# Kernel tuning notes

Hardware: AMD Instinct MI355X
Metric: run time of the kernel (lower is better)

## Reference

```python
import jax, jax.numpy as jnp
import numpy as np

B, N, F, D, H = 4, 2048, 128, 128, 4

def setup_inputs() -> dict:
    key = jax.random.key(0)
    k1, k2, k3, k4 = jax.random.split(key, 4)
    X = jax.random.normal(k1, (B, N, F), dtype=jnp.float32)
    A = jax.random.uniform(k2, (B, N, N), dtype=jnp.float32)
    kernel = jax.random.normal(k3, (F, D), dtype=jnp.float32) * 0.05
    bias = jnp.ones((D,), dtype=jnp.float32)
    attn = jax.random.normal(k4, (H, D, D), dtype=jnp.float32) * 0.05
    return {"X": X, "A": A, "kernel": kernel, "bias": bias, "attn": attn}

def reference(X, A, kernel, bias, attn):
    # Linear projection: [B,N,F] @ [F,D] + bias -> [B,N,D]
    Xp = jnp.einsum('bnf,fd->bnd', X, kernel) + bias
    # Per-head bilinear scores Xp @ attn_h @ Xp^T, batched over heads: [B,H,N,N]
    scores = jnp.einsum('bnd,hde,bme->bhnm', Xp, attn, Xp)
    # Adjacency mask + tanh (fused elementwise)
    Am = jnp.tanh(A[:, None, :, :] * scores)
    # Weighted aggregate per head: [B,H,N,N] @ [B,N,D] -> [B,H,N,D]
    heads = jnp.einsum('bhnm,bmd->bhnd', Am, Xp)
    # Mean over heads, relu
    Xh = jax.nn.relu(jnp.mean(heads, axis=1))
    # Skip connection (shapes match since F == D): relu(Xh + X)
    out = jax.nn.relu(Xh + X)
    return out
```

## Files before the change

### kernel.cpp

```cpp
#include <hip/hip_runtime.h>

#define NB 4
#define NN 2048
#define ND 128
#define NH 4

typedef short short8 __attribute__((ext_vector_type(8)));
typedef short short4v __attribute__((ext_vector_type(4)));
typedef float floatx4 __attribute__((ext_vector_type(4)));

__device__ __forceinline__ short f2bf(float f){
  unsigned u = __float_as_uint(f);
  u += 0x7FFFu + ((u >> 16) & 1u);
  return (short)(u >> 16);
}
__device__ __forceinline__ float bf2f(short s){
  unsigned u = ((unsigned)(unsigned short)s) << 16;
  return __uint_as_float(u);
}

__global__ void k0_transpose(const float* __restrict__ W, const float* __restrict__ attn,
                             short* __restrict__ WT, short* __restrict__ attnT){
  int mat = blockIdx.x;
  const float* src = (mat == 0) ? W : (attn + (mat - 1) * 16384);
  short* dst = (mat == 0) ? WT : (attnT + (mat - 1) * 16384);
  __shared__ short tile[128 * 130];
  int t = threadIdx.x;
  for (int k = 0; k < 64; ++k){
    int idx = k * 256 + t;
    int r = idx >> 7, c = idx & 127;
    tile[c * 130 + r] = f2bf(src[idx]);
  }
  __syncthreads();
  for (int k = 0; k < 8; ++k){
    int g = k * 256 + t;
    int r = g >> 4, c8 = g & 15;
    short8 v;
    #pragma unroll
    for (int j = 0; j < 8; ++j) v[j] = tile[r * 130 + c8 * 8 + j];
    *(short8*)&dst[r * 128 + c8 * 8] = v;
  }
}

__global__ __launch_bounds__(256) void k1_xp(const float* __restrict__ X,
                                             const short* __restrict__ WT,
                                             const float* __restrict__ bias,
                                             short* __restrict__ Xp){
  int bid = blockIdx.x;
  int b = bid >> 5, i0 = (bid & 31) << 6;
  int t = threadIdx.x, w = t >> 6, lane = t & 63, lq = lane >> 4, lc = lane & 15;
  __shared__ __align__(16) short ldsB[16384];
  #pragma unroll
  for (int c = 0; c < 8; ++c){
    int q = c * 256 + t; int fblk = q >> 7; int d = q & 127;
    *(short8*)&ldsB[q * 8] = *(const short8*)&WT[d * 128 + fblk * 8];
  }
  short8 af[4][4];
  #pragma unroll
  for (int ib = 0; ib < 4; ++ib)
    #pragma unroll
    for (int k = 0; k < 4; ++k){
      const float* xp = &X[(b * NN + i0 + ib * 16 + lc) * ND + k * 32 + lq * 8];
      float4 x0 = *(const float4*)xp;
      float4 x1 = *(const float4*)(xp + 4);
      short8 s;
      s[0]=f2bf(x0.x); s[1]=f2bf(x0.y); s[2]=f2bf(x0.z); s[3]=f2bf(x0.w);
      s[4]=f2bf(x1.x); s[5]=f2bf(x1.y); s[6]=f2bf(x1.z); s[7]=f2bf(x1.w);
      af[ib][k] = s;
    }
  __syncthreads();
  floatx4 acc[4][2];
  #pragma unroll
  for (int ib = 0; ib < 4; ++ib)
    #pragma unroll
    for (int eb = 0; eb < 2; ++eb) acc[ib][eb] = (floatx4){0.f, 0.f, 0.f, 0.f};
  #pragma unroll
  for (int eb = 0; eb < 2; ++eb)
    #pragma unroll
    for (int k = 0; k < 4; ++k){
      short8 bf = *(short8*)&ldsB[(k * 4 + lq) * 1024 + (w * 32 + eb * 16 + lc) * 8];
      #pragma unroll
      for (int ib = 0; ib < 4; ++ib)
        acc[ib][eb] = __builtin_amdgcn_mfma_f32_16x16x32_bf16(af[ib][k], bf, acc[ib][eb], 0, 0, 0);
    }
  #pragma unroll
  for (int ib = 0; ib < 4; ++ib)
    #pragma unroll
    for (int eb = 0; eb < 2; ++eb){
      int d = w * 32 + eb * 16 + lc;
      float bv = bias[d];
      #pragma unroll
      for (int r = 0; r < 4; ++r){
        int n = i0 + ib * 16 + lq * 4 + r;
        Xp[(b * NN + n) * ND + d] = f2bf(acc[ib][eb][r] + bv);
      }
    }
}

__global__ void k1b_transpose(const short* __restrict__ Xp, short* __restrict__ XpT){
  int bid = blockIdx.x;
  int b = bid >> 6; int rem = bid & 63;
  int n0 = (rem >> 1) << 6, d0 = (rem & 1) << 6;
  __shared__ short tile[64 * 66];
  int t = threadIdx.x;
  #pragma unroll
  for (int c = 0; c < 2; ++c){
    int g = c * 256 + t; int r = g >> 3, c8 = g & 7;
    short8 v = *(const short8*)&Xp[(b * NN + n0 + r) * ND + d0 + c8 * 8];
    #pragma unroll
    for (int j = 0; j < 8; ++j) tile[(c8 * 8 + j) * 66 + r] = v[j];
  }
  __syncthreads();
  #pragma unroll
  for (int c = 0; c < 2; ++c){
    int g = c * 256 + t; int d = g >> 3, n8 = g & 7;
    short8 v;
    #pragma unroll
    for (int j = 0; j < 8; ++j) v[j] = tile[d * 66 + n8 * 8 + j];
    *(short8*)&XpT[(b * ND + d0 + d) * NN + n0 + n8 * 8] = v;
  }
}

__global__ __launch_bounds__(256) void k2_y(const short* __restrict__ Xp,
                                            const short* __restrict__ attnT,
                                            short* __restrict__ Y){
  int bid = blockIdx.x;
  int it = bid & 31, h = (bid >> 5) & 3, b = bid >> 7;
  int i0 = it << 6;
  int t = threadIdx.x, w = t >> 6, lane = t & 63, lq = lane >> 4, lc = lane & 15;
  __shared__ __align__(16) short ldsB[16384];
  const short* Bsrc = attnT + h * 16384;
  #pragma unroll
  for (int c = 0; c < 8; ++c){
    int q = c * 256 + t; int dblk = q >> 7; int e = q & 127;
    *(short8*)&ldsB[q * 8] = *(const short8*)&Bsrc[e * 128 + dblk * 8];
  }
  short8 af[4][4];
  #pragma unroll
  for (int ib = 0; ib < 4; ++ib)
    #pragma unroll
    for (int k = 0; k < 4; ++k)
      af[ib][k] = *(const short8*)&Xp[(b * NN + i0 + ib * 16 + lc) * ND + k * 32 + lq * 8];
  __syncthreads();
  floatx4 acc[4][2];
  #pragma unroll
  for (int ib = 0; ib < 4; ++ib)
    #pragma unroll
    for (int eb = 0; eb < 2; ++eb) acc[ib][eb] = (floatx4){0.f, 0.f, 0.f, 0.f};
  #pragma unroll
  for (int eb = 0; eb < 2; ++eb)
    #pragma unroll
    for (int k = 0; k < 4; ++k){
      short8 bf = *(short8*)&ldsB[(k * 4 + lq) * 1024 + (w * 32 + eb * 16 + lc) * 8];
      #pragma unroll
      for (int ib = 0; ib < 4; ++ib)
        acc[ib][eb] = __builtin_amdgcn_mfma_f32_16x16x32_bf16(af[ib][k], bf, acc[ib][eb], 0, 0, 0);
    }
  #pragma unroll
  for (int ib = 0; ib < 4; ++ib)
    #pragma unroll
    for (int eb = 0; eb < 2; ++eb){
      int e = w * 32 + eb * 16 + lc;
      #pragma unroll
      for (int r = 0; r < 4; ++r){
        int n = i0 + ib * 16 + lq * 4 + r;
        Y[((b * NH + h) * NN + n) * ND + e] = f2bf(acc[ib][eb][r]);
      }
    }
}

__global__ __launch_bounds__(256, 4) void k3_fused(const short* __restrict__ Xp,
                                                   const short* __restrict__ XpT,
                                                   const short* __restrict__ Y,
                                                   const float* __restrict__ A,
                                                   float* __restrict__ part){
  int bid = blockIdx.x;
  int it = bid & 127, b = (bid >> 7) & 3, ms = bid >> 9;
  int i0 = it << 4;
  int t = threadIdx.x, w = t >> 6, lane = t & 63, lq = lane >> 4, lc = lane & 15;

  __shared__ __align__(16) short ldsPh[2][1024];
  __shared__ __align__(16) short ldsPl[2][1024];

  short8 yf[4][4];
  #pragma unroll
  for (int h = 0; h < 4; ++h)
    #pragma unroll
    for (int k = 0; k < 4; ++k)
      yf[h][k] = *(const short8*)&Y[((b * NH + h) * NN + i0 + lc) * ND + k * 32 + lq * 8];

  floatx4 acc[2];
  acc[0] = (floatx4){0.f,0.f,0.f,0.f};
  acc[1] = (floatx4){0.f,0.f,0.f,0.f};

  const int mbase = ms << 9;
  const int poff = (w * 2 + (lq >> 1)) * 128 + lc * 8 + (lq & 1) * 4;
  const float* arow = &A[(size_t)(b * NN + i0 + lc) * NN];

  floatx4 av = *(const floatx4*)&arow[mbase + w * 16 + lq * 4];

  for (int itn = 0; itn < 8; ++itn){
    int p = itn & 1;
    int m0 = mbase + itn * 64;

    short8 xtf[2][2];
    #pragma unroll
    for (int kb = 0; kb < 2; ++kb)
      #pragma unroll
      for (int db = 0; db < 2; ++db)
        xtf[kb][db] = *(const short8*)&XpT[(b * ND + w * 32 + db * 16 + lc) * NN
                                           + m0 + (kb * 4 + lq) * 8];

    short8 xpf[4];
    const short* xr = Xp + (b * NN + m0 + w * 16 + lc) * ND;
    #pragma unroll
    for (int k = 0; k < 4; ++k) xpf[k] = *(const short8*)&xr[k * 32 + lq * 8];

    floatx4 avn = av;
    if (itn < 7) avn = *(const floatx4*)&arow[m0 + 64 + w * 16 + lq * 4];

    float psum[4] = {0.f, 0.f, 0.f, 0.f};
    #pragma unroll
    for (int h = 0; h < 4; ++h){
      floatx4 S = (floatx4){0.f,0.f,0.f,0.f};
      #pragma unroll
      for (int k = 0; k < 4; ++k)
        S = __builtin_amdgcn_mfma_f32_16x16x32_bf16(xpf[k], yf[h][k], S, 0, 0, 0);
      #pragma unroll
      for (int r = 0; r < 4; ++r){
        float x = av[r] * S[r];
        float e = __builtin_amdgcn_exp2f(x * 2.885390081777926f);
        psum[r] += 1.f - 2.f * __builtin_amdgcn_rcpf(e + 1.f);
      }
    }
    short4v hi4, lo4;
    #pragma unroll
    for (int r = 0; r < 4; ++r){
      float pb = 0.25f * psum[r];
      short h16 = f2bf(pb);
      hi4[r] = h16;
      lo4[r] = f2bf(pb - bf2f(h16));
    }
    *(short4v*)&ldsPh[p][poff] = hi4;
    *(short4v*)&ldsPl[p][poff] = lo4;
    __syncthreads();

    #pragma unroll
    for (int kb = 0; kb < 2; ++kb){
      short8 ph = *(short8*)&ldsPh[p][(kb * 4 + lq) * 128 + lc * 8];
      short8 pl = *(short8*)&ldsPl[p][(kb * 4 + lq) * 128 + lc * 8];
      #pragma unroll
      for (int db = 0; db < 2; ++db){
        acc[db] = __builtin_amdgcn_mfma_f32_16x16x32_bf16(ph, xtf[kb][db], acc[db], 0, 0, 0);
        acc[db] = __builtin_amdgcn_mfma_f32_16x16x32_bf16(pl, xtf[kb][db], acc[db], 0, 0, 0);
      }
    }
    av = avn;
  }
  float* dst = part + (size_t)ms * 1048576 + (b * NN + i0) * ND;
  #pragma unroll
  for (int db = 0; db < 2; ++db)
    #pragma unroll
    for (int r = 0; r < 4; ++r)
      dst[(lq * 4 + r) * ND + w * 32 + db * 16 + lc] = acc[db][r];
}

__global__ void k4_final(const float* __restrict__ part, const float* __restrict__ X,
                         float* __restrict__ out){
  int f = (blockIdx.x * 256 + threadIdx.x) * 4;
  float4 s0 = *(const float4*)(part + f);
  float4 s1 = *(const float4*)(part + 1048576 + f);
  float4 s2 = *(const float4*)(part + 2097152 + f);
  float4 s3 = *(const float4*)(part + 3145728 + f);
  float4 xv = *(const float4*)(X + f);
  float4 o;
  o.x = fmaxf(fmaxf(s0.x + s1.x + s2.x + s3.x, 0.f) + xv.x, 0.f);
  o.y = fmaxf(fmaxf(s0.y + s1.y + s2.y + s3.y, 0.f) + xv.y, 0.f);
  o.z = fmaxf(fmaxf(s0.z + s1.z + s2.z + s3.z, 0.f) + xv.z, 0.f);
  o.w = fmaxf(fmaxf(s0.w + s1.w + s2.w + s3.w, 0.f) + xv.w, 0.f);
  *(float4*)(out + f) = o;
}

extern "C" void kernel_launch(void* const* d_in, const int* in_sizes, int n_in,
                              void* d_out, int out_size, void* d_ws, size_t ws_size,
                              hipStream_t stream) {
  const float* X    = (const float*)d_in[0];
  const float* A    = (const float*)d_in[1];
  const float* W    = (const float*)d_in[2];
  const float* bias = (const float*)d_in[3];
  const float* attn = (const float*)d_in[4];
  float* out = (float*)d_out;

  const size_t OFF_XP    = 0;
  const size_t OFF_XPT   = (size_t)2 << 20;
  const size_t OFF_Y     = (size_t)4 << 20;
  const size_t OFF_PART  = (size_t)12 << 20;
  const size_t OFF_WT    = (size_t)28 << 20;
  const size_t OFF_ATTNT = OFF_WT + 32768;
  const size_t NEED = OFF_ATTNT + 131072;
  if (ws_size < NEED) return;

  char* ws = (char*)d_ws;
  short* Xp    = (short*)(ws + OFF_XP);
  short* XpT   = (short*)(ws + OFF_XPT);
  short* Y     = (short*)(ws + OFF_Y);
  float* part  = (float*)(ws + OFF_PART);
  short* WT    = (short*)(ws + OFF_WT);
  short* attnT = (short*)(ws + OFF_ATTNT);

  k0_transpose<<<5, 256, 0, stream>>>(W, attn, WT, attnT);
  k1_xp<<<128, 256, 0, stream>>>(X, WT, bias, Xp);
  k1b_transpose<<<256, 256, 0, stream>>>(Xp, XpT);
  k2_y<<<512, 256, 0, stream>>>(Xp, attnT, Y);
  k3_fused<<<2048, 256, 0, stream>>>(Xp, XpT, Y, A, part);
  k4_final<<<1024, 256, 0, stream>>>(part, X, out);
}
```

Measured before the change: 196.9 us.

## Remove per-iteration barrier by giving each wave all output columns

```diff
diff --git a/kernel.cpp b/kernel.cpp
--- a/kernel.cpp
+++ b/kernel.cpp
@@ -179,53 +179,51 @@
   int i0 = it << 4;
   int t = threadIdx.x, w = t >> 6, lane = t & 63, lq = lane >> 4, lc = lane & 15;
 
-  __shared__ __align__(16) short ldsPh[2][1024];
-  __shared__ __align__(16) short ldsPl[2][1024];
-
-  short8 yf[4][4];
-  #pragma unroll
-  for (int h = 0; h < 4; ++h)
-    #pragma unroll
-    for (int k = 0; k < 4; ++k)
-      yf[h][k] = *(const short8*)&Y[((b * NH + h) * NN + i0 + lc) * ND + k * 32 + lq * 8];
-
-  floatx4 acc[2];
-  acc[0] = (floatx4){0.f,0.f,0.f,0.f};
-  acc[1] = (floatx4){0.f,0.f,0.f,0.f};
+  __shared__ __align__(16) char smem[32768];
+
+  #pragma unroll
+  for (int c = 0; c < 4; ++c){
+    int slot = c * 256 + t;
+    int h = slot >> 8, i = (slot >> 4) & 15, d8 = slot & 15;
+    short8 v = *(const short8*)&Y[((b * NH + h) * NN + i0 + i) * ND + d8 * 8];
+    *(short8*)(smem + h * 4096 + i * 256 + ((d8 ^ (i & 7)) << 4)) = v;
+  }
+  __syncthreads();
+
+  floatx4 acc[8];
+  #pragma unroll
+  for (int dt = 0; dt < 8; ++dt) acc[dt] = (floatx4){0.f,0.f,0.f,0.f};
 
   const int mbase = ms << 9;
-  const int poff = (w * 2 + (lq >> 1)) * 128 + lc * 8 + (lq & 1) * 4;
   const float* arow = &A[(size_t)(b * NN + i0 + lc) * NN];
 
   floatx4 av = *(const floatx4*)&arow[mbase + w * 16 + lq * 4];
 
   for (int itn = 0; itn < 8; ++itn){
-    int p = itn & 1;
-    int m0 = mbase + itn * 64;
-
-    short8 xtf[2][2];
-    #pragma unroll
-    for (int kb = 0; kb < 2; ++kb)
-      #pragma unroll
-      for (int db = 0; db < 2; ++db)
-        xtf[kb][db] = *(const short8*)&XpT[(b * ND + w * 32 + db * 16 + lc) * NN
-                                           + m0 + (kb * 4 + lq) * 8];
+    int m0 = mbase + itn * 64 + w * 16;
 
     short8 xpf[4];
-    const short* xr = Xp + (b * NN + m0 + w * 16 + lc) * ND;
+    const short* xr = Xp + (b * NN + m0 + lc) * ND;
     #pragma unroll
     for (int k = 0; k < 4; ++k) xpf[k] = *(const short8*)&xr[k * 32 + lq * 8];
 
+    short4v xt[8];
+    #pragma unroll
+    for (int dt = 0; dt < 8; ++dt)
+      xt[dt] = *(const short4v*)&XpT[(size_t)(b * ND + dt * 16 + lc) * NN + m0 + lq * 4];
+
     floatx4 avn = av;
-    if (itn < 7) avn = *(const floatx4*)&arow[m0 + 64 + w * 16 + lq * 4];
+    if (itn < 7) avn = *(const floatx4*)&arow[m0 + 64 + lq * 4];
 
     float psum[4] = {0.f, 0.f, 0.f, 0.f};
     #pragma unroll
     for (int h = 0; h < 4; ++h){
       floatx4 S = (floatx4){0.f,0.f,0.f,0.f};
       #pragma unroll
-      for (int k = 0; k < 4; ++k)
-        S = __builtin_amdgcn_mfma_f32_16x16x32_bf16(xpf[k], yf[h][k], S, 0, 0, 0);
+      for (int k = 0; k < 4; ++k){
+        short8 yf = *(short8*)(smem + h * 4096 + lc * 256 + (((k * 4 + lq) ^ (lc & 7)) << 4));
+        S = __builtin_amdgcn_mfma_f32_16x16x32_bf16(xpf[k], yf, S, 0, 0, 0);
+      }
       #pragma unroll
       for (int r = 0; r < 4; ++r){
         float x = av[r] * S[r];
@@ -233,6 +231,7 @@
         psum[r] += 1.f - 2.f * __builtin_amdgcn_rcpf(e + 1.f);
       }
     }
+
     short4v hi4, lo4;
     #pragma unroll
     for (int r = 0; r < 4; ++r){
@@ -241,28 +240,29 @@
       hi4[r] = h16;
       lo4[r] = f2bf(pb - bf2f(h16));
     }
-    *(short4v*)&ldsPh[p][poff] = hi4;
-    *(short4v*)&ldsPl[p][poff] = lo4;
-    __syncthreads();
-
-    #pragma unroll
-    for (int kb = 0; kb < 2; ++kb){
-      short8 ph = *(short8*)&ldsPh[p][(kb * 4 + lq) * 128 + lc * 8];
-      short8 pl = *(short8*)&ldsPl[p][(kb * 4 + lq) * 128 + lc * 8];
-      #pragma unroll
-      for (int db = 0; db < 2; ++db){
-        acc[db] = __builtin_amdgcn_mfma_f32_16x16x32_bf16(ph, xtf[kb][db], acc[db], 0, 0, 0);
-        acc[db] = __builtin_amdgcn_mfma_f32_16x16x32_bf16(pl, xtf[kb][db], acc[db], 0, 0, 0);
-      }
+
+    #pragma unroll
+    for (int dt = 0; dt < 8; ++dt){
+      acc[dt] = __builtin_amdgcn_mfma_f32_16x16x16bf16_1k(hi4, xt[dt], acc[dt], 0, 0, 0);
+      acc[dt] = __builtin_amdgcn_mfma_f32_16x16x16bf16_1k(lo4, xt[dt], acc[dt], 0, 0, 0);
     }
     av = avn;
   }
-  float* dst = part + (size_t)ms * 1048576 + (b * NN + i0) * ND;
-  #pragma unroll
-  for (int db = 0; db < 2; ++db)
+
+  __syncthreads();
+  float* red = (float*)smem;
+  #pragma unroll
+  for (int dt = 0; dt < 8; ++dt)
     #pragma unroll
     for (int r = 0; r < 4; ++r)
-      dst[(lq * 4 + r) * ND + w * 32 + db * 16 + lc] = acc[db][r];
+      red[w * 2048 + (lq * 4 + r) * 128 + dt * 16 + lc] = acc[dt][r];
+  __syncthreads();
+  float* dst = part + (size_t)ms * 1048576 + (size_t)(b * NN + i0) * ND;
+  #pragma unroll
+  for (int j = 0; j < 8; ++j){
+    int idx = j * 256 + t;
+    dst[idx] = red[idx] + red[2048 + idx] + red[4096 + idx] + red[6144 + idx];
+  }
 }
 
 __global__ void k4_final(const float* __restrict__ part, const float* __restrict__ X,
```

Measured after the change: 275.7 us. 1.4x slower.
